# Performance work log

Hardware: AMD Instinct MI355X
Metric: run time of the kernel (lower is better)

Reference implementation:

```python
import jax, jax.numpy as jnp
import numpy as np

B, T, S = 32, 200, 256          # batch, decoder steps, encoder (memory) length
L = 512                          # latent_dims
U = 2 * L                        # LSTM units / attention units / attention_layer_size
E = 512                          # encoder memory feature dim
M = 80                           # mel_bins


def setup_inputs() -> dict:
    key = jax.random.key(0)
    ks = jax.random.split(key, 16)
    s = 0.05
    inputs = jax.random.normal(ks[0], (B, T, M), jnp.float32)
    memory = jax.random.normal(ks[1], (B, S, E), jnp.float32)
    # pre-net: Dense(2L, relu) -> Dropout -> Dense(L, relu) -> Dropout
    W1 = jax.random.normal(ks[2], (M, 2 * L), jnp.float32) * s
    b1 = jnp.zeros((2 * L,), jnp.float32)
    W2 = jax.random.normal(ks[3], (2 * L, L), jnp.float32) * s
    b2 = jnp.zeros((L,), jnp.float32)
    # LSTMCell(2L): input = concat(prenet_out [L], attention [U=2L]) -> 3L
    Wx = jax.random.normal(ks[4], (3 * L, 4 * U), jnp.float32) * s
    Wh = jax.random.normal(ks[5], (U, 4 * U), jnp.float32) * s
    b_lstm = jnp.zeros((4 * U,), jnp.float32)
    # Bahdanau attention (units=U): memory_layer, query_layer (no bias), score vector v
    Wm = jax.random.normal(ks[6], (E, U), jnp.float32) * s
    Wq = jax.random.normal(ks[7], (U, U), jnp.float32) * s
    v_att = jax.random.normal(ks[8], (U,), jnp.float32) * s
    # attention_layer (Dense, no bias): concat(cell_output [U], context [E]) -> U
    Wa = jax.random.normal(ks[9], (U + E, U), jnp.float32) * s
    # output projection to mel bins
    Wp = jax.random.normal(ks[10], (U, M), jnp.float32) * s
    bp = jnp.zeros((M,), jnp.float32)
    return dict(inputs=inputs, memory=memory, W1=W1, b1=b1, W2=W2, b2=b2,
                Wx=Wx, Wh=Wh, b_lstm=b_lstm, Wm=Wm, Wq=Wq, v_att=v_att,
                Wa=Wa, Wp=Wp, bp=bp)


def reference(inputs, memory, W1, b1, W2, b2, Wx, Wh, b_lstm, Wm, Wq, v_att, Wa, Wp, bp):
    # pre-net (inference: dropout is identity)
    x = jax.nn.relu(inputs @ W1 + b1)
    x = jax.nn.relu(x @ W2 + b2)                       # [B,T,L]
    keys = memory @ Wm                                 # precomputed attention keys [B,S,U]

    def step(carry, xt):
        h, c, attn = carry
        cell_in = jnp.concatenate([xt, attn], axis=-1)  # [B, 3L]
        z = cell_in @ Wx + h @ Wh + b_lstm              # [B, 4U]
        i, f, g, o = jnp.split(z, 4, axis=-1)
        c_new = jax.nn.sigmoid(f) * c + jax.nn.sigmoid(i) * jnp.tanh(g)
        h_new = jax.nn.sigmoid(o) * jnp.tanh(c_new)
        # Bahdanau additive attention
        q = h_new @ Wq                                  # [B,U]
        score = jnp.einsum('u,bsu->bs', v_att, jnp.tanh(keys + q[:, None, :]))
        align = jax.nn.softmax(score, axis=-1)          # [B,S]
        ctx = jnp.einsum('bs,bse->be', align, memory)   # [B,E]
        attn_new = jnp.concatenate([h_new, ctx], axis=-1) @ Wa  # [B,U]
        return (h_new, c_new, attn_new), attn_new

    init = (jnp.zeros((B, U), x.dtype), jnp.zeros((B, U), x.dtype), jnp.zeros((B, U), x.dtype))
    xs = jnp.swapaxes(x, 0, 1)                          # [T,B,L]
    (h, c, attn), ys = jax.lax.scan(step, init, xs)
    outs = jnp.swapaxes(ys, 0, 1)                       # [B,T,U]
    mel = outs @ Wp + bp                                # [B,T,M]
    return (mel, h, c, attn)
```

## Files before the change

### kernel.cpp

```cpp
#include <hip/hip_runtime.h>


typedef unsigned short us16;
typedef unsigned int u32;
typedef unsigned long long u64;
typedef __attribute__((ext_vector_type(8))) short bf16x8;
typedef __attribute__((ext_vector_type(4))) float f32x4;

#define MFMA16 __builtin_amdgcn_mfma_f32_16x16x32_bf16
#define AGT __HIP_MEMORY_SCOPE_AGENT

__device__ __forceinline__ us16 f2bf(float f){
  u32 u = __builtin_bit_cast(u32, f);
  u += 0x7fffu + ((u >> 16) & 1u);
  return (us16)(u >> 16);
}
__device__ __forceinline__ float bf2f(us16 h){
  return __builtin_bit_cast(float, ((u32)h) << 16);
}
__device__ __forceinline__ float h2f(us16 u){
  _Float16 h = __builtin_bit_cast(_Float16, u); return (float)h;
}
__device__ __forceinline__ us16 f2h(float f){
  _Float16 h = (_Float16)f; return __builtin_bit_cast(us16, h);
}
__device__ __forceinline__ void split3(float v, us16& s0, us16& s1, us16& s2){
  s0 = f2bf(v); float r = v - bf2f(s0);
  s1 = f2bf(r); r -= bf2f(s1);
  s2 = f2bf(r);
}
__device__ __forceinline__ float tanh_fast(float x){
  float e = __expf(-2.f * fmaxf(x, -40.f));
  return (1.f - e) / (1.f + e);
}

__device__ __forceinline__ u32 aload32(const u32* p){
  return __hip_atomic_load(p, __ATOMIC_RELAXED, AGT);
}
__device__ __forceinline__ u64 aload64(const u64* p){
  return __hip_atomic_load(p, __ATOMIC_RELAXED, AGT);
}
__device__ __forceinline__ void astore16(us16* p, us16 v){
  __hip_atomic_store(p, v, __ATOMIC_RELAXED, AGT);
}
__device__ __forceinline__ void astoref(float* p, float v){
  __hip_atomic_store(p, v, __ATOMIC_RELAXED, AGT);
}
__device__ __forceinline__ void sigflag(u32* p, u32 v){
  __hip_atomic_store(p, v, __ATOMIC_RELAXED, AGT);
}
__device__ __forceinline__ void aaddf(float* p, float v){
  __hip_atomic_fetch_add(p, v, __ATOMIC_RELAXED, AGT);
}
__device__ __forceinline__ bf16x8 ld16(const us16* p){
  return *(const bf16x8*)p;
}
__device__ __forceinline__ float4 aloadf4(const float* p){
  union { u64 u[2]; float4 f; } t;
  const u64* q = (const u64*)p;
  t.u[0] = aload64(q); t.u[1] = aload64(q + 1);
  return t.f;
}
__device__ __forceinline__ bf16x8 pin_reg(bf16x8 v){
  f32x4 t = __builtin_bit_cast(f32x4, v);
  asm volatile("" : "+v"(t));
  return __builtin_bit_cast(bf16x8, t);
}
__device__ __forceinline__ void f32_frag3(const float* p, float rs,
                                          bf16x8& f0, bf16x8& f1, bf16x8& f2){
  float4 t0 = *(const float4*)p;
  float4 t1 = *(const float4*)(p + 4);
  float tf[8] = {t0.x, t0.y, t0.z, t0.w, t1.x, t1.y, t1.z, t1.w};
#pragma unroll
  for (int i = 0; i < 8; ++i){
    float v = tf[i] * rs;
    us16 s0, s1, s2; split3(v, s0, s1, s2);
    f0[i] = (short)s0; f1[i] = (short)s1; f2[i] = (short)s2;
  }
}

#define OFF_WTA    0ull
#define OFF_WQT    50331648ull
#define OFF_X2P    56623104ull
#define OFF_KEYH   76283904ull
#define OFF_KEYL   93061120ull
#define OFF_X1     76283904ull
#define OFF_HIST   109838336ull
#define OFF_HPR    129597440ull
#define OFF_UCR    169115648ull
#define OFF_SR     182288384ull
#define OFF_QB     182314112ull
#define OFF_CB     182445184ull
#define OFF_HF     182576256ull
#define OFF_WAPN   182707328ull
#define OFF_BPERM  182953088ull
#define OFF_FLG    182969472ull
#define TOTAL_WS   183018624ull

#define WTPL 8388608ull
#define WQPL 1048576ull
#define X2PL 3276800ull

__global__ void k_zero_init(u32* hpr0, float* ucr, float* sr, float* cbuf, u32* flg){
  u32 id = blockIdx.x * 256u + threadIdx.x;
  const u32 gs = 65536u;
  for (u32 i = id; i < 49152u;   i += gs) hpr0[i] = 0u;
  for (u32 i = id; i < 3293184u; i += gs) ucr[i]  = 0.f;
  for (u32 i = id; i < 6432u;    i += gs) sr[i]   = (i < 32u) ? 1.f : 0.f;
  for (u32 i = id; i < 32768u;   i += gs) cbuf[i] = 0.f;
  for (u32 i = id; i < 12288u;   i += gs) flg[i]  = 0u;
}

__global__ void k_bperm(const float* __restrict__ bl, float* __restrict__ bpm){
  int c = blockIdx.x * 256 + threadIdx.x;
  if (c < 4096) bpm[((c & 1023) << 2) | (c >> 10)] = bl[c];
}

__global__ void k_transp3(const float* __restrict__ src, us16* __restrict__ dst,
                          int srows, int scols, int ldd, long long pstride, int perm){
  __shared__ float tile[32][33];
  int bx = blockIdx.x * 32, by = blockIdx.y * 32;
  int tx = threadIdx.x & 31, ty = threadIdx.x >> 5;
#pragma unroll
  for (int i = 0; i < 4; ++i){
    int r = by + ty + i * 8, c = bx + tx;
    tile[ty + i * 8][tx] = (r < srows && c < scols) ? src[(size_t)r * scols + c] : 0.f;
  }
  __syncthreads();
#pragma unroll
  for (int i = 0; i < 4; ++i){
    int c = bx + ty + i * 8;
    int r = by + tx;
    if (c < scols && r < srows){
      int oc = perm ? (((c & 1023) << 2) | (c >> 10)) : c;
      float v = tile[tx][ty + i * 8];
      us16 s0, s1, s2; split3(v, s0, s1, s2);
      size_t base = (size_t)oc * ldd + r;
      dst[base] = s0; dst[(size_t)pstride + base] = s1; dst[2ull * pstride + base] = s2;
    }
  }
}

template<int NP, int AF, int BF>
__global__ void __launch_bounds__(256)
k_gemm3(const void* __restrict__ Ap, const void* __restrict__ Bp, void* __restrict__ outp,
        int M, int N, int K, int mode, const float* __restrict__ aux, int ldd){
  __shared__ us16 At[NP][128][72];
  __shared__ us16 Bt[NP][64][72];
  const int tid = threadIdx.x, wv = tid >> 6, lane = tid & 63;
  const int r0 = lane & 15, kg = lane >> 4;
  const int rb = blockIdx.x * 128, cb = blockIdx.y * 64;
  f32x4 acc[2][4];
#pragma unroll
  for (int a = 0; a < 2; ++a)
#pragma unroll
    for (int b = 0; b < 4; ++b) acc[a][b] = (f32x4){0.f, 0.f, 0.f, 0.f};

  const int nkt = (K + 63) >> 6;
  for (int kt = 0; kt < nkt; ++kt){
    const int kb = kt * 64;
    for (int e = tid; e < 8192; e += 256){
      int r = e >> 6, k = e & 63, ga = rb + r, gk = kb + k;
      bool ok = (ga < M) && (gk < K);
      if constexpr (AF){
        float v = ok ? ((const float*)Ap)[(size_t)ga * K + gk] : 0.f;
        us16 s0, s1, s2; split3(v, s0, s1, s2);
        At[0][r][k] = s0;
        if constexpr (NP == 3){ At[1][r][k] = s1; At[2][r][k] = s2; }
      } else {
        At[0][r][k] = ok ? ((const us16*)Ap)[(size_t)ga * K + gk] : (us16)0;
      }
    }
    for (int e = tid; e < 4096; e += 256){
      int kr = e >> 6, c = e & 63, gk = kb + kr, gc = cb + c;
      bool ok = (gk < K) && (gc < N);
      if constexpr (BF){
        float v = ok ? ((const float*)Bp)[(size_t)gk * N + gc] : 0.f;
        us16 s0, s1, s2; split3(v, s0, s1, s2);
        Bt[0][c][kr] = s0;
        if constexpr (NP == 3){ Bt[1][c][kr] = s1; Bt[2][c][kr] = s2; }
      } else {
        Bt[0][c][kr] = ok ? ((const us16*)Bp)[(size_t)gk * N + gc] : (us16)0;
      }
    }
    __syncthreads();
#pragma unroll
    for (int kk = 0; kk < 64; kk += 32){
      bf16x8 af[NP][2];
#pragma unroll
      for (int p = 0; p < NP; ++p){
        af[p][0] = *(const bf16x8*)&At[p][wv * 32 + r0][kk + kg * 8];
        af[p][1] = *(const bf16x8*)&At[p][wv * 32 + 16 + r0][kk + kg * 8];
      }
#pragma unroll
      for (int cf = 0; cf < 4; ++cf){
        bf16x8 bv[NP];
#pragma unroll
        for (int p = 0; p < NP; ++p) bv[p] = *(const bf16x8*)&Bt[p][cf * 16 + r0][kk + kg * 8];
#pragma unroll
        for (int rf = 0; rf < 2; ++rf){
          acc[rf][cf] = MFMA16(af[0][rf], bv[0], acc[rf][cf], 0, 0, 0);
          if constexpr (NP == 3){
            acc[rf][cf] = MFMA16(af[0][rf], bv[1], acc[rf][cf], 0, 0, 0);
            acc[rf][cf] = MFMA16(af[1][rf], bv[0], acc[rf][cf], 0, 0, 0);
            acc[rf][cf] = MFMA16(af[0][rf], bv[2], acc[rf][cf], 0, 0, 0);
            acc[rf][cf] = MFMA16(af[1][rf], bv[1], acc[rf][cf], 0, 0, 0);
            acc[rf][cf] = MFMA16(af[2][rf], bv[0], acc[rf][cf], 0, 0, 0);
          }
        }
      }
    }
    __syncthreads();
  }
  us16* o16 = (us16*)outp; float* of = (float*)outp;
#pragma unroll
  for (int rf = 0; rf < 2; ++rf)
#pragma unroll
    for (int cf = 0; cf < 4; ++cf)
#pragma unroll
      for (int i = 0; i < 4; ++i){
        int r = rb + wv * 32 + rf * 16 + kg * 4 + i;
        int c = cb + cf * 16 + r0;
        if (r >= M || c >= N) continue;
        float v = acc[rf][cf][i];
        if (mode == 0){
          of[(size_t)r * ldd + c] = fmaxf(v + aux[c], 0.f);
        } else if (mode == 1){
          v = fmaxf(v + aux[c], 0.f);
          us16 s0, s1, s2; split3(v, s0, s1, s2);
          size_t b2 = (size_t)r * ldd + c;
          o16[b2] = s0; o16[X2PL + b2] = s1; o16[2 * X2PL + b2] = s2;
        } else if (mode == 2){
          us16 hh = f2h(v); float rem = v - h2f(hh); us16 hl = f2h(rem);
          size_t b2 = (size_t)r * 1024 + c;
          o16[b2] = hh; o16[WTPL + b2] = hl;
        } else if (mode == 3){
          float w = v + (r < 1024 ? aux[(size_t)r * 4096 + c] : 0.f);
          int pc = (c & 1023) * 4 + (c >> 10);
          us16 s0, s1, s2; split3(w, s0, s1, s2);
          size_t b2 = (size_t)pc * 2048 + 512 + r;
          o16[b2] = s0; o16[WTPL + b2] = s1; o16[2 * WTPL + b2] = s2;
        } else if (mode == 4){
          o16[(size_t)r * ldd + c] = f2bf(v);
        } else if (mode == 5){
          of[((size_t)(r & 31) * 200 + (r >> 5)) * 80 + c] = v + aux[c];
        } else {
          of[(size_t)r * ldd + c] = v;
        }
      }
}

struct CoopA {
  const us16 *wta, *wqt, *x2p, *kh, *kl;
  const float *mem, *vatt, *bperm;
  us16 *hist, *hpr;
  float *ucr, *sr, *qb, *cbuf, *hf32;
  u32 *flg;
};

#define DRAIN asm volatile("s_waitcnt vmcnt(0)" ::: "memory")

__global__ void __launch_bounds__(512, 1) k_coop(CoopA a){
  __shared__ us16 khi[32][1024];
  __shared__ us16 klo[32][1024];
  __shared__ float zp[8][512];
  __shared__ float esc[32];
  __shared__ float rs_lds[32];

  __builtin_amdgcn_fence(__ATOMIC_ACQUIRE, "agent");

  const int tid = threadIdx.x, blk = blockIdx.x;
  const int wv = tid >> 6, lane = tid & 63;
  const int r0 = lane & 15, kg = lane >> 4;
  const int cb_b = blk >> 3, cb_s0 = (blk & 7) * 32;
  const int colbase = blk * 16;
  const int u0 = lane * 16;
  u32* hfl = a.flg;
  u32* qfl = a.flg + 4096;
  u32* cfl = a.flg + 8192;

  bf16x8 wr[8][3];
#pragma unroll
  for (int ks = 0; ks < 8; ++ks){
    const size_t wb = (size_t)(colbase + r0) * 2048 + (size_t)wv * 256 + ks * 32 + kg * 8;
#pragma unroll
    for (int p = 0; p < 3; ++p)
      wr[ks][p] = pin_reg(*(const bf16x8*)&a.wta[(size_t)p * WTPL + wb]);
  }

  {
    const size_t kbase = ((size_t)(cb_b * 256 + cb_s0)) * 1024;
    for (int i = tid; i < 4096; i += 512){
      int r = i >> 7, c8 = (i & 127) * 8;
      *(bf16x8*)&khi[r][c8] = *(const bf16x8*)&a.kh[kbase + (size_t)r * 1024 + c8];
      *(bf16x8*)&klo[r][c8] = *(const bf16x8*)&a.kl[kbase + (size_t)r * 1024 + c8];
    }
  }
  __syncthreads();

  for (int t = 0; t < 200; ++t){
    const u32 ep = (u32)(t + 1);
    {
      if (tid < 32) rs_lds[tid] = 1.f / a.sr[(size_t)t * 32 + tid];
      __syncthreads();
      if (tid < 64){
        int flat = blk * 64 + tid;
        int b = flat >> 9, e = flat & 511;
        float v = a.ucr[(size_t)t * 16384 + flat];
        a.hist[(size_t)(t * 32 + b) * 1536 + 1024 + e] = f2bf(v * rs_lds[b]);
      }
      f32x4 acc0 = (f32x4){0.f,0.f,0.f,0.f}, acc1 = acc0;
#pragma unroll
      for (int ks = 0; ks < 8; ++ks){
        const int k0 = wv * 256 + ks * 32;
        const int kf = k0 + kg * 8;
        bf16x8 w0 = wr[ks][0], w1 = wr[ks][1], w2 = wr[ks][2];
        bf16x8 a00, a01, a02, a10, a11, a12;
        if (wv < 2){
          const size_t xb0 = ((size_t)r0 * 200 + t) * 512 + kf;
          const size_t xb1 = ((size_t)(r0 + 16) * 200 + t) * 512 + kf;
          a00 = *(const bf16x8*)&a.x2p[xb0];
          a01 = *(const bf16x8*)&a.x2p[X2PL + xb0];
          a02 = *(const bf16x8*)&a.x2p[2 * X2PL + xb0];
          a10 = *(const bf16x8*)&a.x2p[xb1];
          a11 = *(const bf16x8*)&a.x2p[X2PL + xb1];
          a12 = *(const bf16x8*)&a.x2p[2 * X2PL + xb1];
        } else if (wv < 6){
          const int hk = kf - 512;
          const us16* hb = a.hpr + (size_t)t * 98304;
          a00 = ld16(&hb[(size_t)r0 * 1024 + hk]);
          a01 = ld16(&hb[32768 + (size_t)r0 * 1024 + hk]);
          a02 = ld16(&hb[65536 + (size_t)r0 * 1024 + hk]);
          a10 = ld16(&hb[(size_t)(r0 + 16) * 1024 + hk]);
          a11 = ld16(&hb[32768 + (size_t)(r0 + 16) * 1024 + hk]);
          a12 = ld16(&hb[65536 + (size_t)(r0 + 16) * 1024 + hk]);
        } else {
          const int ek = kf - 1536;
          const float* up = a.ucr + (size_t)t * 16384 + (size_t)r0 * 512 + ek;
          f32_frag3(up,        rs_lds[r0],      a00, a01, a02);
          f32_frag3(up + 8192, rs_lds[r0 + 16], a10, a11, a12);
        }
        acc0 = MFMA16(a00, w0, acc0, 0,0,0); acc0 = MFMA16(a00, w1, acc0, 0,0,0);
        acc0 = MFMA16(a01, w0, acc0, 0,0,0); acc0 = MFMA16(a00, w2, acc0, 0,0,0);
        acc0 = MFMA16(a01, w1, acc0, 0,0,0); acc0 = MFMA16(a02, w0, acc0, 0,0,0);
        acc1 = MFMA16(a10, w0, acc1, 0,0,0); acc1 = MFMA16(a10, w1, acc1, 0,0,0);
        acc1 = MFMA16(a11, w0, acc1, 0,0,0); acc1 = MFMA16(a10, w2, acc1, 0,0,0);
        acc1 = MFMA16(a11, w1, acc1, 0,0,0); acc1 = MFMA16(a12, w0, acc1, 0,0,0);
      }
#pragma unroll
      for (int i = 0; i < 4; ++i){
        zp[wv][(kg * 4 + i) * 16 + r0]      = acc0[i];
        zp[wv][(16 + kg * 4 + i) * 16 + r0] = acc1[i];
      }
      __syncthreads();
      float z = 0.f;
#pragma unroll
      for (int w = 0; w < 8; ++w) z += zp[w][tid];
      z += a.bperm[colbase + (tid & 15)];
      __syncthreads();
      zp[0][tid] = z;
      __syncthreads();
      if (tid < 128){
        int b = tid >> 2, ul = tid & 3, u = blk * 4 + ul;
        float zi = zp[0][b * 16 + ul * 4 + 0];
        float zf = zp[0][b * 16 + ul * 4 + 1];
        float zg = zp[0][b * 16 + ul * 4 + 2];
        float zo = zp[0][b * 16 + ul * 4 + 3];
        float co = a.cbuf[b * 1024 + u];
        float cn = (1.f / (1.f + expf(-zf))) * co + (1.f / (1.f + expf(-zi))) * tanhf(zg);
        float hn = (1.f / (1.f + expf(-zo))) * tanhf(cn);
        a.cbuf[b * 1024 + u] = cn;
        a.hf32[b * 1024 + u] = hn;
        us16 s0, s1, s2; split3(hn, s0, s1, s2);
        a.hist[((size_t)(t + 1) * 32 + b) * 1536 + u] = s0;
        us16* hb = a.hpr + (size_t)(t + 1) * 98304;
        astore16(&hb[b * 1024 + u], s0);
        astore16(&hb[32768 + b * 1024 + u], s1);
        astore16(&hb[65536 + b * 1024 + u], s2);
      }
    }
    DRAIN;
    __syncthreads();
    if (tid == 0) sigflag(&hfl[blk * 16], ep);

    if (blk < 64){
      if (tid < 256) while (aload32(&hfl[tid * 16]) < ep) __builtin_amdgcn_s_sleep(1);
      __syncthreads();
      f32x4 acc0 = (f32x4){0.f,0.f,0.f,0.f}, acc1 = acc0;
#pragma unroll
      for (int ks = 0; ks < 4; ++ks){
        const int kf = wv * 128 + ks * 32 + kg * 8;
        const size_t wb = (size_t)(colbase + r0) * 1024 + kf;
        bf16x8 w0 = *(const bf16x8*)&a.wqt[wb];
        bf16x8 w1 = *(const bf16x8*)&a.wqt[WQPL + wb];
        bf16x8 w2 = *(const bf16x8*)&a.wqt[2 * WQPL + wb];
        const us16* hb = a.hpr + (size_t)(t + 1) * 98304;
        bf16x8 a00 = ld16(&hb[(size_t)r0 * 1024 + kf]);
        bf16x8 a01 = ld16(&hb[32768 + (size_t)r0 * 1024 + kf]);
        bf16x8 a02 = ld16(&hb[65536 + (size_t)r0 * 1024 + kf]);
        bf16x8 a10 = ld16(&hb[(size_t)(r0 + 16) * 1024 + kf]);
        bf16x8 a11 = ld16(&hb[32768 + (size_t)(r0 + 16) * 1024 + kf]);
        bf16x8 a12 = ld16(&hb[65536 + (size_t)(r0 + 16) * 1024 + kf]);
        acc0 = MFMA16(a00, w0, acc0, 0,0,0); acc0 = MFMA16(a00, w1, acc0, 0,0,0);
        acc0 = MFMA16(a01, w0, acc0, 0,0,0); acc0 = MFMA16(a00, w2, acc0, 0,0,0);
        acc0 = MFMA16(a01, w1, acc0, 0,0,0); acc0 = MFMA16(a02, w0, acc0, 0,0,0);
        acc1 = MFMA16(a10, w0, acc1, 0,0,0); acc1 = MFMA16(a10, w1, acc1, 0,0,0);
        acc1 = MFMA16(a11, w0, acc1, 0,0,0); acc1 = MFMA16(a10, w2, acc1, 0,0,0);
        acc1 = MFMA16(a11, w1, acc1, 0,0,0); acc1 = MFMA16(a12, w0, acc1, 0,0,0);
      }
#pragma unroll
      for (int i = 0; i < 4; ++i){
        zp[wv][(kg * 4 + i) * 16 + r0]      = acc0[i];
        zp[wv][(16 + kg * 4 + i) * 16 + r0] = acc1[i];
      }
      __syncthreads();
      float q = 0.f;
#pragma unroll
      for (int w = 0; w < 8; ++w) q += zp[w][tid];
      astoref(&a.qb[(size_t)(tid >> 4) * 1024 + colbase + (tid & 15)], q);
      DRAIN;
      __syncthreads();
      if (tid == 0) sigflag(&qfl[blk * 16], ep);
    }
    if (tid < 64) while (aload32(&qfl[tid * 16]) < ep) __builtin_amdgcn_s_sleep(1);
    __syncthreads();

    {
      float qv[16], vv[16];
      {
        const float* qp = a.qb + (size_t)cb_b * 1024 + u0;
        float4 q0 = aloadf4(qp), q1 = aloadf4(qp + 4);
        float4 q2 = aloadf4(qp + 8), q3 = aloadf4(qp + 12);
        qv[0]=q0.x; qv[1]=q0.y; qv[2]=q0.z; qv[3]=q0.w;
        qv[4]=q1.x; qv[5]=q1.y; qv[6]=q1.z; qv[7]=q1.w;
        qv[8]=q2.x; qv[9]=q2.y; qv[10]=q2.z; qv[11]=q2.w;
        qv[12]=q3.x; qv[13]=q3.y; qv[14]=q3.z; qv[15]=q3.w;
        float4 v0 = *(const float4*)(a.vatt + u0);
        float4 v1 = *(const float4*)(a.vatt + u0 + 4);
        float4 v2 = *(const float4*)(a.vatt + u0 + 8);
        float4 v3 = *(const float4*)(a.vatt + u0 + 12);
        vv[0]=v0.x; vv[1]=v0.y; vv[2]=v0.z; vv[3]=v0.w;
        vv[4]=v1.x; vv[5]=v1.y; vv[6]=v1.z; vv[7]=v1.w;
        vv[8]=v2.x; vv[9]=v2.y; vv[10]=v2.z; vv[11]=v2.w;
        vv[12]=v3.x; vv[13]=v3.y; vv[14]=v3.z; vv[15]=v3.w;
      }
#pragma unroll
      for (int m = 0; m < 4; ++m){
        const int sl = wv * 4 + m;
        bf16x8 h0 = *(const bf16x8*)&khi[sl][u0];
        bf16x8 h1 = *(const bf16x8*)&khi[sl][u0 + 8];
        bf16x8 l0 = *(const bf16x8*)&klo[sl][u0];
        bf16x8 l1 = *(const bf16x8*)&klo[sl][u0 + 8];
        float part = 0.f;
#pragma unroll
        for (int j = 0; j < 8; ++j){
          float kva = h2f((us16)h0[j]) + h2f((us16)l0[j]);
          part += vv[j] * tanh_fast(kva + qv[j]);
          float kvb = h2f((us16)h1[j]) + h2f((us16)l1[j]);
          part += vv[8 + j] * tanh_fast(kvb + qv[8 + j]);
        }
#pragma unroll
        for (int off = 32; off; off >>= 1) part += __shfl_xor(part, off);
        if (lane == 0) esc[sl] = __expf(part);
      }
      __syncthreads();
      if (tid == 0){
        float bs = 0.f;
#pragma unroll
        for (int i = 0; i < 32; ++i) bs += esc[i];
        aaddf(&a.sr[(size_t)(t + 1) * 32 + cb_b], bs);
      }
      {
        float ac0 = 0.f, ac1 = 0.f, ac2 = 0.f, ac3 = 0.f;
        const float* mrow = a.mem + ((size_t)(cb_b * 256 + cb_s0)) * 512 + tid;
#pragma unroll
        for (int j = 0; j < 32; j += 4){
          ac0 += esc[j]     * mrow[(size_t)j * 512];
          ac1 += esc[j + 1] * mrow[(size_t)(j + 1) * 512];
          ac2 += esc[j + 2] * mrow[(size_t)(j + 2) * 512];
          ac3 += esc[j + 3] * mrow[(size_t)(j + 3) * 512];
        }
        aaddf(&a.ucr[(size_t)(t + 1) * 16384 + cb_b * 512 + tid], (ac0 + ac1) + (ac2 + ac3));
      }
    }
    DRAIN;
    __syncthreads();
    if (tid == 0) sigflag(&cfl[blk * 16], ep);
    if (tid < 256) while (aload32(&cfl[tid * 16]) < ep) __builtin_amdgcn_s_sleep(1);
    __syncthreads();
  }

  {
    if (tid < 32) rs_lds[tid] = 1.f / a.sr[(size_t)200 * 32 + tid];
    __syncthreads();
    if (tid < 64){
      int flat = blk * 64 + tid;
      int b = flat >> 9, e = flat & 511;
      float v = a.ucr[(size_t)200 * 16384 + flat];
      a.hist[(size_t)(200 * 32 + b) * 1536 + 1024 + e] = f2bf(v * rs_lds[b]);
    }
  }
}

__global__ void k_copy_hc(const float* __restrict__ h, const float* __restrict__ c,
                          float* __restrict__ out){
  int i = blockIdx.x * 256 + threadIdx.x;
  if (i < 32768){
    out[512000 + i] = h[i];
    out[544768 + i] = c[i];
  }
}

extern "C" void kernel_launch(void* const* d_in, const int* in_sizes, int n_in,
                              void* d_out, int out_size, void* d_ws, size_t ws_size,
                              hipStream_t stream){
  const float* inputs = (const float*)d_in[0];
  const float* memory = (const float*)d_in[1];
  const float* W1     = (const float*)d_in[2];
  const float* b1     = (const float*)d_in[3];
  const float* W2     = (const float*)d_in[4];
  const float* b2     = (const float*)d_in[5];
  const float* Wx     = (const float*)d_in[6];
  const float* Wh     = (const float*)d_in[7];
  const float* b_lstm = (const float*)d_in[8];
  const float* Wm     = (const float*)d_in[9];
  const float* Wq     = (const float*)d_in[10];
  const float* v_att  = (const float*)d_in[11];
  const float* Wa     = (const float*)d_in[12];
  const float* Wp     = (const float*)d_in[13];
  const float* bp     = (const float*)d_in[14];
  float* out = (float*)d_out;
  char* ws = (char*)d_ws;
  if (ws_size < TOTAL_WS) return;

  us16* WTA    = (us16*)(ws + OFF_WTA);
  us16* WQT    = (us16*)(ws + OFF_WQT);
  us16* X2P    = (us16*)(ws + OFF_X2P);
  us16* KEYH   = (us16*)(ws + OFF_KEYH);
  float* X1    = (float*)(ws + OFF_X1);
  us16* HIST   = (us16*)(ws + OFF_HIST);
  us16* HPR    = (us16*)(ws + OFF_HPR);
  float* UCR   = (float*)(ws + OFF_UCR);
  float* SR    = (float*)(ws + OFF_SR);
  float* QB    = (float*)(ws + OFF_QB);
  float* CB    = (float*)(ws + OFF_CB);
  float* HF    = (float*)(ws + OFF_HF);
  us16* WAPN   = (us16*)(ws + OFF_WAPN);
  float* BPM   = (float*)(ws + OFF_BPERM);
  u32*  FLG    = (u32*)(ws + OFF_FLG);

  k_zero_init<<<256, 256, 0, stream>>>((u32*)HPR, UCR, SR, CB, FLG);
  k_bperm<<<16, 256, 0, stream>>>(b_lstm, BPM);
  k_transp3<<<dim3(32, 32), 256, 0, stream>>>(Wq, WQT, 1024, 1024, 1024, (long long)WQPL, 0);
  k_transp3<<<dim3(128, 16), 256, 0, stream>>>(Wx, WTA, 512, 4096, 2048, (long long)WTPL, 1);

  k_gemm3<3,1,1><<<dim3(12, 64), 256, 0, stream>>>(Wa, Wx + (size_t)512 * 4096, WTA,
                                                   1536, 4096, 1024, 3, Wh, 0);
  k_gemm3<3,1,1><<<dim3(12, 2), 256, 0, stream>>>(Wa, Wp, WAPN, 1536, 80, 1024, 4, nullptr, 80);
  k_gemm3<3,1,1><<<dim3(50, 16), 256, 0, stream>>>(inputs, W1, X1, 6400, 1024, 80, 0, b1, 1024);
  k_gemm3<3,1,1><<<dim3(50, 8), 256, 0, stream>>>(X1, W2, X2P, 6400, 512, 1024, 1, b2, 512);
  k_gemm3<3,1,1><<<dim3(64, 16), 256, 0, stream>>>(memory, Wm, KEYH, 8192, 1024, 512, 2, nullptr, 1024);

  CoopA ca;
  ca.wta = WTA; ca.wqt = WQT; ca.x2p = X2P; ca.kh = KEYH; ca.kl = KEYH + WTPL;
  ca.mem = memory; ca.vatt = v_att; ca.bperm = BPM;
  ca.hist = HIST; ca.hpr = HPR; ca.ucr = UCR; ca.sr = SR;
  ca.qb = QB; ca.cbuf = CB; ca.hf32 = HF; ca.flg = FLG;
  void* args[] = {(void*)&ca};
  hipLaunchCooperativeKernel((const void*)k_coop, dim3(256), dim3(512), args, 0, stream);

  k_gemm3<1,0,0><<<dim3(50, 2), 256, 0, stream>>>(HIST + (size_t)32 * 1536, WAPN, out,
                                                  6400, 80, 1536, 5, bp, 0);
  k_gemm3<1,0,1><<<dim3(1, 16), 256, 0, stream>>>(HIST + (size_t)200 * 32 * 1536, Wa,
                                                  out + 577536, 32, 1024, 1536, 6, nullptr, 1024);
  k_copy_hc<<<128, 256, 0, stream>>>(HF, CB, out);
}
```

Measured before the change: 12.98 ms.

## Replace flag-based inter-block sync with centralized barrier and defer history packing

```diff
diff --git a/kernel.cpp b/kernel.cpp
--- a/kernel.cpp
+++ b/kernel.cpp
@@ -32,6 +32,9 @@
 __device__ __forceinline__ float tanh_fast(float x){
   float e = __expf(-2.f * fmaxf(x, -40.f));
   return (1.f - e) / (1.f + e);
+}
+__device__ __forceinline__ float sigf(float x){
+  return 1.f / (1.f + __expf(-x));
 }
 
 __device__ __forceinline__ u32 aload32(const u32* p){
@@ -94,21 +97,21 @@
 #define OFF_HF     182576256ull
 #define OFF_WAPN   182707328ull
 #define OFF_BPERM  182953088ull
-#define OFF_FLG    182969472ull
-#define TOTAL_WS   183018624ull
+#define OFF_ARR    182969472ull
+#define TOTAL_WS   182987776ull
 
 #define WTPL 8388608ull
 #define WQPL 1048576ull
 #define X2PL 3276800ull
 
-__global__ void k_zero_init(u32* hpr0, float* ucr, float* sr, float* cbuf, u32* flg){
+__global__ void k_zero_init(u32* hpr0, float* ucr, float* sr, float* cbuf, u32* arr){
   u32 id = blockIdx.x * 256u + threadIdx.x;
   const u32 gs = 65536u;
   for (u32 i = id; i < 49152u;   i += gs) hpr0[i] = 0u;
   for (u32 i = id; i < 3293184u; i += gs) ucr[i]  = 0.f;
   for (u32 i = id; i < 6432u;    i += gs) sr[i]   = (i < 32u) ? 1.f : 0.f;
   for (u32 i = id; i < 32768u;   i += gs) cbuf[i] = 0.f;
-  for (u32 i = id; i < 12288u;   i += gs) flg[i]  = 0u;
+  for (u32 i = id; i < 4352u;    i += gs) arr[i]  = 0u;
 }
 
 __global__ void k_bperm(const float* __restrict__ bl, float* __restrict__ bpm){
@@ -250,15 +253,32 @@
       }
 }
 
+__device__ __forceinline__ void gbar2(u32* arr, u32 ep, int tid, int blk){
+  asm volatile("s_waitcnt vmcnt(0)" ::: "memory");
+  __syncthreads();
+  if (blk == 0){
+    if (tid > 0 && tid < 256)
+      while (aload32(&arr[tid * 16]) < ep) __builtin_amdgcn_s_sleep(1);
+    __syncthreads();
+    if (tid == 0) sigflag(&arr[4096], ep);
+    __syncthreads();
+  } else {
+    if (tid == 0){
+      sigflag(&arr[blk * 16], ep);
+      while (aload32(&arr[4096]) < ep) __builtin_amdgcn_s_sleep(1);
+      __builtin_amdgcn_sched_barrier(0);
+    }
+    __syncthreads();
+  }
+}
+
 struct CoopA {
   const us16 *wta, *wqt, *x2p, *kh, *kl;
   const float *mem, *vatt, *bperm;
-  us16 *hist, *hpr;
+  us16 *hpr;
   float *ucr, *sr, *qb, *cbuf, *hf32;
-  u32 *flg;
+  u32 *arr;
 };
-
-#define DRAIN asm volatile("s_waitcnt vmcnt(0)" ::: "memory")
 
 __global__ void __launch_bounds__(512, 1) k_coop(CoopA a){
   __shared__ us16 khi[32][1024];
@@ -275,9 +295,6 @@
   const int cb_b = blk >> 3, cb_s0 = (blk & 7) * 32;
   const int colbase = blk * 16;
   const int u0 = lane * 16;
-  u32* hfl = a.flg;
-  u32* qfl = a.flg + 4096;
-  u32* cfl = a.flg + 8192;
 
   bf16x8 wr[8][3];
 #pragma unroll
@@ -298,22 +315,15 @@
   }
   __syncthreads();
 
+  u32 ep = 0;
   for (int t = 0; t < 200; ++t){
-    const u32 ep = (u32)(t + 1);
     {
       if (tid < 32) rs_lds[tid] = 1.f / a.sr[(size_t)t * 32 + tid];
       __syncthreads();
-      if (tid < 64){
-        int flat = blk * 64 + tid;
-        int b = flat >> 9, e = flat & 511;
-        float v = a.ucr[(size_t)t * 16384 + flat];
-        a.hist[(size_t)(t * 32 + b) * 1536 + 1024 + e] = f2bf(v * rs_lds[b]);
-      }
       f32x4 acc0 = (f32x4){0.f,0.f,0.f,0.f}, acc1 = acc0;
 #pragma unroll
       for (int ks = 0; ks < 8; ++ks){
-        const int k0 = wv * 256 + ks * 32;
-        const int kf = k0 + kg * 8;
+        const int kf = wv * 256 + ks * 32 + kg * 8;
         bf16x8 w0 = wr[ks][0], w1 = wr[ks][1], w2 = wr[ks][2];
         bf16x8 a00, a01, a02, a10, a11, a12;
         if (wv < 2){
@@ -367,25 +377,20 @@
         float zg = zp[0][b * 16 + ul * 4 + 2];
         float zo = zp[0][b * 16 + ul * 4 + 3];
         float co = a.cbuf[b * 1024 + u];
-        float cn = (1.f / (1.f + expf(-zf))) * co + (1.f / (1.f + expf(-zi))) * tanhf(zg);
-        float hn = (1.f / (1.f + expf(-zo))) * tanhf(cn);
+        float cn = sigf(zf) * co + sigf(zi) * tanh_fast(zg);
+        float hn = sigf(zo) * tanh_fast(cn);
         a.cbuf[b * 1024 + u] = cn;
         a.hf32[b * 1024 + u] = hn;
         us16 s0, s1, s2; split3(hn, s0, s1, s2);
-        a.hist[((size_t)(t + 1) * 32 + b) * 1536 + u] = s0;
         us16* hb = a.hpr + (size_t)(t + 1) * 98304;
         astore16(&hb[b * 1024 + u], s0);
         astore16(&hb[32768 + b * 1024 + u], s1);
         astore16(&hb[65536 + b * 1024 + u], s2);
       }
     }
-    DRAIN;
-    __syncthreads();
-    if (tid == 0) sigflag(&hfl[blk * 16], ep);
+    gbar2(a.arr, ++ep, tid, blk);
 
     if (blk < 64){
-      if (tid < 256) while (aload32(&hfl[tid * 16]) < ep) __builtin_amdgcn_s_sleep(1);
-      __syncthreads();
       f32x4 acc0 = (f32x4){0.f,0.f,0.f,0.f}, acc1 = acc0;
 #pragma unroll
       for (int ks = 0; ks < 4; ++ks){
@@ -418,12 +423,8 @@
 #pragma unroll
       for (int w = 0; w < 8; ++w) q += zp[w][tid];
       astoref(&a.qb[(size_t)(tid >> 4) * 1024 + colbase + (tid & 15)], q);
-      DRAIN;
-      __syncthreads();
-      if (tid == 0) sigflag(&qfl[blk * 16], ep);
-    }
-    if (tid < 64) while (aload32(&qfl[tid * 16]) < ep) __builtin_amdgcn_s_sleep(1);
-    __syncthreads();
+    }
+    gbar2(a.arr, ++ep, tid, blk);
 
     {
       float qv[16], vv[16];
@@ -483,22 +484,20 @@
         aaddf(&a.ucr[(size_t)(t + 1) * 16384 + cb_b * 512 + tid], (ac0 + ac1) + (ac2 + ac3));
       }
     }
-    DRAIN;
-    __syncthreads();
-    if (tid == 0) sigflag(&cfl[blk * 16], ep);
-    if (tid < 256) while (aload32(&cfl[tid * 16]) < ep) __builtin_amdgcn_s_sleep(1);
-    __syncthreads();
-  }
-
-  {
-    if (tid < 32) rs_lds[tid] = 1.f / a.sr[(size_t)200 * 32 + tid];
-    __syncthreads();
-    if (tid < 64){
-      int flat = blk * 64 + tid;
-      int b = flat >> 9, e = flat & 511;
-      float v = a.ucr[(size_t)200 * 16384 + flat];
-      a.hist[(size_t)(200 * 32 + b) * 1536 + 1024 + e] = f2bf(v * rs_lds[b]);
-    }
+    gbar2(a.arr, ++ep, tid, blk);
+  }
+}
+
+__global__ void k_hist(const us16* __restrict__ hpr, const float* __restrict__ ucr,
+                       const float* __restrict__ sr, us16* __restrict__ hist){
+  int row = blockIdx.x;
+  int t = row >> 5, b = row & 31;
+  float rs = 1.f / sr[(size_t)t * 32 + b];
+  for (int c = threadIdx.x; c < 1536; c += 256){
+    us16 v;
+    if (c < 1024) v = hpr[(size_t)t * 98304 + b * 1024 + c];
+    else          v = f2bf(ucr[(size_t)t * 16384 + b * 512 + (c - 1024)] * rs);
+    hist[(size_t)row * 1536 + c] = v;
   }
 }
 
@@ -547,9 +546,9 @@
   float* HF    = (float*)(ws + OFF_HF);
   us16* WAPN   = (us16*)(ws + OFF_WAPN);
   float* BPM   = (float*)(ws + OFF_BPERM);
-  u32*  FLG    = (u32*)(ws + OFF_FLG);
-
-  k_zero_init<<<256, 256, 0, stream>>>((u32*)HPR, UCR, SR, CB, FLG);
+  u32*  ARR    = (u32*)(ws + OFF_ARR);
+
+  k_zero_init<<<256, 256, 0, stream>>>((u32*)HPR, UCR, SR, CB, ARR);
   k_bperm<<<16, 256, 0, stream>>>(b_lstm, BPM);
   k_transp3<<<dim3(32, 32), 256, 0, stream>>>(Wq, WQT, 1024, 1024, 1024, (long long)WQPL, 0);
   k_transp3<<<dim3(128, 16), 256, 0, stream>>>(Wx, WTA, 512, 4096, 2048, (long long)WTPL, 1);
@@ -564,11 +563,12 @@
   CoopA ca;
   ca.wta = WTA; ca.wqt = WQT; ca.x2p = X2P; ca.kh = KEYH; ca.kl = KEYH + WTPL;
   ca.mem = memory; ca.vatt = v_att; ca.bperm = BPM;
-  ca.hist = HIST; ca.hpr = HPR; ca.ucr = UCR; ca.sr = SR;
-  ca.qb = QB; ca.cbuf = CB; ca.hf32 = HF; ca.flg = FLG;
+  ca.hpr = HPR; ca.ucr = UCR; ca.sr = SR;
+  ca.qb = QB; ca.cbuf = CB; ca.hf32 = HF; ca.arr = ARR;
   void* args[] = {(void*)&ca};
   hipLaunchCooperativeKernel((const void*)k_coop, dim3(256), dim3(512), args, 0, stream);
 
+  k_hist<<<6432, 256, 0, stream>>>(HPR, UCR, SR, HIST);
   k_gemm3<1,0,0><<<dim3(50, 2), 256, 0, stream>>>(HIST + (size_t)32 * 1536, WAPN, out,
                                                   6400, 80, 1536, 5, bp, 0);
   k_gemm3<1,0,1><<<dim3(1, 16), 256, 0, stream>>>(HIST + (size_t)200 * 32 * 1536, Wa,
```

After: 12.64 ms. 1.03x faster.
